# Kernel optimization log

Hardware: AMD Instinct MI355X
Metric: run time of the kernel (lower is better)

Reference implementation:

```python
import jax, jax.numpy as jnp
import numpy as np

D = 1024
H = 16
HD = D // H  # 64


def setup_inputs() -> dict:
    key = jax.random.key(0)
    k1, k2, k3 = jax.random.split(key, 3)
    x = jax.random.normal(k1, (2, 2048, D), dtype=jnp.float32)
    # fused QKV projection weight [d, 3d] and output projection [d, d], no bias
    Wqkv = jax.random.normal(k2, (D, 3 * D), dtype=jnp.float32) * (1.0 / np.sqrt(D))
    Wo = jax.random.normal(k3, (D, D), dtype=jnp.float32) * (1.0 / np.sqrt(D))
    return {"x": x, "Wqkv": Wqkv, "Wo": Wo}


def reference(x, Wqkv, Wo):
    b, t, d = x.shape
    qkv = x @ Wqkv  # [b, t, 3d]
    q, k, v = jnp.split(qkv, 3, axis=-1)
    # [b, t, d] -> [b, h, t, hd]
    def heads(z):
        return z.reshape(b, t, H, HD).transpose(0, 2, 1, 3)
    q, k, v = heads(q), heads(k), heads(v)
    scale = 1.0 / np.sqrt(HD)
    att = jnp.einsum('bhqd,bhkd->bhqk', q, k) * scale  # [b, h, t, t]
    att = jax.nn.softmax(att, axis=-1)
    y = jnp.einsum('bhqk,bhkd->bhqd', att, v)  # [b, h, t, hd]
    y = y.transpose(0, 2, 1, 3).reshape(b, t, d)  # [b, t, d]
    return y @ Wo
```

## Files before the change

### kernel.cpp

```cpp
#include <hip/hip_runtime.h>
#include <hip/hip_bf16.h>

#define D_MODEL 1024
#define NHEADS  16
#define HD      64
#define BATCH   2
#define SEQ     2048
#define NTOK    (BATCH * SEQ)

typedef __attribute__((ext_vector_type(8))) short bf16x8;
typedef __attribute__((ext_vector_type(4))) float f32x4;

#if __has_builtin(__builtin_amdgcn_exp2f)
#define EXP2F(x) __builtin_amdgcn_exp2f(x)
#else
#define EXP2F(x) exp2f(x)
#endif

static __device__ __forceinline__ short f2bf(float f) {
    union { float f; unsigned u; } x; x.f = f;
    unsigned r = (x.u + 0x7fffu + ((x.u >> 16) & 1u)) >> 16;
    return (short)r;
}

static __device__ __forceinline__ unsigned pk_bf16(float a, float b) {
    __hip_bfloat162 h2 = __float22bfloat162_rn(make_float2(a, b));
    union { __hip_bfloat162 h; unsigned u; } c; c.h = h2;
    return c.u;
}

static __device__ __forceinline__ void gl_lds16(const short* g, short* l) {
    __builtin_amdgcn_global_load_lds((const __attribute__((address_space(1))) void*)g,
                                     (__attribute__((address_space(3))) void*)l,
                                     16, 0, 0);
}

__global__ __launch_bounds__(256) void prep_kernel(const float* __restrict__ x,
                                                   short* __restrict__ x_bf,
                                                   const float* __restrict__ Wqkv,
                                                   short* __restrict__ WqkvT,
                                                   const float* __restrict__ Wo,
                                                   short* __restrict__ WoT,
                                                   float cexp) {
    int bid = blockIdx.x;
    int tid = threadIdx.x;

    if (bid < 4096) {
        int i = bid * 256 + tid;
        float4 v = ((const float4*)x)[i];
        short4 o;
        o.x = f2bf(v.x); o.y = f2bf(v.y); o.z = f2bf(v.z); o.w = f2bf(v.w);
        ((short4*)x_bf)[i] = o;
        return;
    }

    __shared__ float tile[32][33];
    const float* in; short* out; int R, C, slimit; float sc; int bx, by;
    if (bid < 4096 + 3072) {
        int idx = bid - 4096;
        in = Wqkv; out = WqkvT; R = D_MODEL; C = 3 * D_MODEL;
        slimit = D_MODEL; sc = cexp;
        bx = idx % 96; by = idx / 96;
    } else {
        int idx = bid - 7168;
        in = Wo; out = WoT; R = D_MODEL; C = D_MODEL;
        slimit = 0; sc = 1.0f;
        bx = idx % 32; by = idx / 32;
    }
    int bc = bx * 32, br = by * 32;
    int tx = tid & 31, ty = tid >> 5;
    #pragma unroll
    for (int i = 0; i < 32; i += 8)
        tile[ty + i][tx] = in[(long)(br + ty + i) * C + bc + tx];
    __syncthreads();
    #pragma unroll
    for (int i = 0; i < 32; i += 8) {
        int orow = bc + ty + i;
        float v = tile[tx][ty + i];
        if (orow < slimit) v *= sc;
        out[(long)orow * R + br + tx] = f2bf(v);
    }
}

__global__ __launch_bounds__(256) void gemm_out(const short* __restrict__ A,
                                                const short* __restrict__ BT,
                                                float* __restrict__ C,
                                                int M, int N, int K) {
    __shared__ short As[2][128 * 32];
    __shared__ short Bs[2][64 * 32];

    int tid  = threadIdx.x;
    int lane = tid & 63;
    int w    = tid >> 6;
    int quad = lane >> 4;
    int l16  = lane & 15;

    int m_blk = blockIdx.y * 128, n_blk = blockIdx.x * 64;

    const short* Ag = A  + (long)(m_blk + w * 32 + (lane >> 2)) * K + (lane & 3) * 8;
    const short* Bg = BT + (long)(n_blk + w * 16 + (lane >> 2)) * K + (lane & 3) * 8;
    short* As0 = &As[0][(w * 32) * 32];
    short* As1 = &As[1][(w * 32) * 32];
    short* Bs0 = &Bs[0][(w * 16) * 32];
    short* Bs1 = &Bs[1][(w * 16) * 32];

    f32x4 acc[2][4] = {};

    for (int k0 = 0; k0 < K; k0 += 64) {
        __syncthreads();
        gl_lds16(Ag + k0,               As0);
        gl_lds16(Ag + 16 * K + k0,      As0 + 16 * 32);
        gl_lds16(Ag + k0 + 32,          As1);
        gl_lds16(Ag + 16 * K + k0 + 32, As1 + 16 * 32);
        gl_lds16(Bg + k0,               Bs0);
        gl_lds16(Bg + k0 + 32,          Bs1);
        __syncthreads();

        #pragma unroll
        for (int kk = 0; kk < 2; kk++) {
            bf16x8 a[2], b[4];
            #pragma unroll
            for (int i = 0; i < 2; i++)
                a[i] = *(const bf16x8*)&As[kk][(w * 32 + i * 16 + l16) * 32 + quad * 8];
            #pragma unroll
            for (int j = 0; j < 4; j++)
                b[j] = *(const bf16x8*)&Bs[kk][(j * 16 + l16) * 32 + quad * 8];
            #pragma unroll
            for (int i = 0; i < 2; i++)
                #pragma unroll
                for (int j = 0; j < 4; j++)
                    acc[i][j] = __builtin_amdgcn_mfma_f32_16x16x32_bf16(a[i], b[j], acc[i][j], 0, 0, 0);
        }
    }

    #pragma unroll
    for (int i = 0; i < 2; i++)
        #pragma unroll
        for (int j = 0; j < 4; j++)
            #pragma unroll
            for (int r = 0; r < 4; r++) {
                int row = m_blk + w * 32 + i * 16 + quad * 4 + r;
                int col = n_blk + j * 16 + l16;
                C[(long)row * N + col] = acc[i][j][r];
            }
}

__global__ __launch_bounds__(256) void gemm_qkv(const short* __restrict__ A,
                                                const short* __restrict__ BT,
                                                short* __restrict__ Qb,
                                                short* __restrict__ Kt2,
                                                short* __restrict__ Vt2) {
    const int K = 1024;
    __shared__ union {
        struct { short As[2][128 * 32]; short Bs[2][128 * 32]; } g;
        short Tl[4][64][72];
    } sh;

    int tid  = threadIdx.x;
    int lane = tid & 63;
    int w    = tid >> 6;
    int quad = lane >> 4;
    int l16  = lane & 15;

    int bid = blockIdx.y * 24 + blockIdx.x;
    int xcd = bid & 7;
    int pos = bid >> 3;
    int nb  = xcd * 3 + (pos % 3);
    int mb  = pos / 3;

    int m_blk = mb * 128, n_blk = nb * 128;
    int mh = (w >> 1) * 64, nh = (w & 1) * 64;

    int sel = nb >> 3;
    int ncol0 = n_blk - sel * 1024;

    const short* Ag = A  + (long)(m_blk + w * 32 + (lane >> 2)) * K + (lane & 3) * 8;
    const short* Bg = BT + (long)(n_blk + w * 32 + (lane >> 2)) * K + (lane & 3) * 8;
    short* As0 = &sh.g.As[0][(w * 32) * 32];
    short* As1 = &sh.g.As[1][(w * 32) * 32];
    short* Bs0 = &sh.g.Bs[0][(w * 32) * 32];
    short* Bs1 = &sh.g.Bs[1][(w * 32) * 32];

    f32x4 acc[4][4] = {};

    for (int k0 = 0; k0 < K; k0 += 64) {
        __syncthreads();
        gl_lds16(Ag + k0,               As0);
        gl_lds16(Ag + 16 * K + k0,      As0 + 16 * 32);
        gl_lds16(Ag + k0 + 32,          As1);
        gl_lds16(Ag + 16 * K + k0 + 32, As1 + 16 * 32);
        gl_lds16(Bg + k0,               Bs0);
        gl_lds16(Bg + 16 * K + k0,      Bs0 + 16 * 32);
        gl_lds16(Bg + k0 + 32,          Bs1);
        gl_lds16(Bg + 16 * K + k0 + 32, Bs1 + 16 * 32);
        __syncthreads();

        #pragma unroll
        for (int kk = 0; kk < 2; kk++) {
            bf16x8 a[4], b[4];
            #pragma unroll
            for (int i = 0; i < 4; i++)
                a[i] = *(const bf16x8*)&sh.g.As[kk][(mh + i * 16 + l16) * 32 + quad * 8];
            #pragma unroll
            for (int j = 0; j < 4; j++)
                b[j] = *(const bf16x8*)&sh.g.Bs[kk][(nh + j * 16 + l16) * 32 + quad * 8];
            #pragma unroll
            for (int i = 0; i < 4; i++)
                #pragma unroll
                for (int j = 0; j < 4; j++)
                    acc[i][j] = __builtin_amdgcn_mfma_f32_16x16x32_bf16(a[i], b[j], acc[i][j], 0, 0, 0);
        }
    }

    __syncthreads();

    #pragma unroll
    for (int i = 0; i < 4; i++)
        #pragma unroll
        for (int j = 0; j < 4; j++)
            #pragma unroll
            for (int r = 0; r < 4; r++)
                sh.Tl[w][i * 16 + quad * 4 + r][j * 16 + l16] = f2bf(acc[i][j][r]);

    int R0q = m_blk + mh;
    if (sel == 0) {
        long qbase = (long)R0q * 1024 + (ncol0 + nh);
        #pragma unroll
        for (int ch = 0; ch < 8; ch++) {
            int row  = ch * 8 + (lane >> 3);
            int col0 = (lane & 7) * 8;
            *(bf16x8*)(Qb + qbase + (long)row * 1024 + col0) =
                *(const bf16x8*)&sh.Tl[w][row][col0];
        }
    } else {
        int b2 = R0q >> 11;
        int t  = (R0q & 2047) >> 6;
        int h  = (ncol0 + nh) >> 6;
        long obase = (long)(b2 * 16 + h) * (SEQ * 64) + (long)t * 4096;
        short* outT = (sel == 1) ? Kt2 : Vt2;
        if (sel == 1) {
            #pragma unroll
            for (int ch = 0; ch < 8; ch++) {
                int o = lane * 64 + ch * 8;
                int u = o >> 9, qd = (o >> 7) & 3, l = (o >> 3) & 15;
                int row = (u >> 2) * 32 + ((u >> 1) & 1) * 16 + l;
                int col = (u & 1) * 32 + qd * 8;
                *(bf16x8*)(outT + obase + o) = *(const bf16x8*)&sh.Tl[w][row][col];
            }
        } else {
            #pragma unroll
            for (int ch = 0; ch < 8; ch++) {
                int o = lane * 64 + ch * 8;
                int c = o >> 11, j2 = (o >> 9) & 3, qd = (o >> 7) & 3, l = (o >> 3) & 15;
                int hd = j2 * 16 + l;
                bf16x8 ov;
                #pragma unroll
                for (int jj = 0; jj < 8; jj++) {
                    int s = c * 32 + qd * 8 + jj;
                    int key = (s >> 2) + ((s & 3) << 4);
                    ov[jj] = sh.Tl[w][key][hd];
                }
                *(bf16x8*)(outT + obase + o) = ov;
            }
        }
    }
}

__global__ __launch_bounds__(256, 4) void flash_attn(const short* __restrict__ Qb,
                                                     const short* __restrict__ Kt2,
                                                     const short* __restrict__ Vt2,
                                                     short* __restrict__ y) {
    int tid  = threadIdx.x;
    int lane = tid & 63;
    int w    = tid >> 6;
    int quad = lane >> 4;
    int l16  = lane & 15;
    int qsel = w & 1;
    int ksel = w >> 1;

    int bh = blockIdx.y;
    int b  = bh >> 4;
    int h  = bh & 15;
    int qw = blockIdx.x * 64 + qsel * 32;

    __shared__ union {
        short Ps[4][32 * 72];
        float Mg[2][64][41];
    } sh;
    short* PsW = &sh.Ps[w][0];

    const short* Qrow = Qb + ((long)b * SEQ + qw + l16) * 1024 + h * 64;
    bf16x8 aQ[2][2];
    #pragma unroll
    for (int m = 0; m < 2; m++)
        #pragma unroll
        for (int c = 0; c < 2; c++)
            aQ[m][c] = *(const bf16x8*)(Qrow + (long)(m * 16) * 1024 + c * 32 + quad * 8);

    const short* Ktb = Kt2 + (long)bh * (SEQ * 64) + (long)ksel * 16 * 4096;
    const short* Vtb = Vt2 + (long)bh * (SEQ * 64) + (long)ksel * 16 * 4096;

    f32x4 O[2][4] = {};
    f32x4 Lacc[2] = {};
    bf16x8 ones;
    #pragma unroll
    for (int i = 0; i < 8; i++) ones[i] = (short)0x3F80;

    for (int t = 0; t < 16; t++) {
        const short* Kt = Ktb + t * 4096;
        const short* Vt = Vtb + t * 4096;

        bf16x8 kf[8];
        #pragma unroll
        for (int u = 0; u < 8; u++) kf[u] = *(const bf16x8*)(Kt + u * 512 + lane * 8);

        f32x4 z[2][4];
        #pragma unroll
        for (int m = 0; m < 2; m++)
            #pragma unroll
            for (int kc = 0; kc < 4; kc++) {
                f32x4 zz = {};
                zz = __builtin_amdgcn_mfma_f32_16x16x32_bf16(aQ[m][0], kf[2 * kc],     zz, 0, 0, 0);
                z[m][kc] = __builtin_amdgcn_mfma_f32_16x16x32_bf16(aQ[m][1], kf[2 * kc + 1], zz, 0, 0, 0);
            }

        bf16x8 vf[8];
        #pragma unroll
        for (int u = 0; u < 8; u++) vf[u] = *(const bf16x8*)(Vt + u * 512 + lane * 8);

        #pragma unroll
        for (int m = 0; m < 2; m++)
            #pragma unroll
            for (int r = 0; r < 4; r++) {
                unsigned d0 = pk_bf16(EXP2F(z[m][0][r]), EXP2F(z[m][1][r]));
                unsigned d1 = pk_bf16(EXP2F(z[m][2][r]), EXP2F(z[m][3][r]));
                unsigned long long dd = ((unsigned long long)d1 << 32) | d0;
                *(unsigned long long*)((unsigned*)PsW + (m * 16 + quad * 4 + r) * 36 + 2 * l16) = dd;
            }

        #pragma unroll
        for (int c = 0; c < 2; c++) {
            bf16x8 aP0 = *(const bf16x8*)(PsW + (l16) * 72      + c * 32 + quad * 8);
            bf16x8 aP1 = *(const bf16x8*)(PsW + (16 + l16) * 72 + c * 32 + quad * 8);
            Lacc[0] = __builtin_amdgcn_mfma_f32_16x16x32_bf16(aP0, ones, Lacc[0], 0, 0, 0);
            Lacc[1] = __builtin_amdgcn_mfma_f32_16x16x32_bf16(aP1, ones, Lacc[1], 0, 0, 0);
            #pragma unroll
            for (int j = 0; j < 4; j++) {
                O[0][j] = __builtin_amdgcn_mfma_f32_16x16x32_bf16(aP0, vf[c * 4 + j], O[0][j], 0, 0, 0);
                O[1][j] = __builtin_amdgcn_mfma_f32_16x16x32_bf16(aP1, vf[c * 4 + j], O[1][j], 0, 0, 0);
            }
        }
    }

    __syncthreads();
    if (ksel) {
        float* mg = &sh.Mg[qsel][lane][0];
        #pragma unroll
        for (int m = 0; m < 2; m++)
            #pragma unroll
            for (int j = 0; j < 4; j++)
                #pragma unroll
                for (int r = 0; r < 4; r++)
                    mg[m * 16 + j * 4 + r] = O[m][j][r];
        #pragma unroll
        for (int m = 0; m < 2; m++)
            #pragma unroll
            for (int r = 0; r < 4; r++)
                mg[32 + m * 4 + r] = Lacc[m][r];
    }
    __syncthreads();
    if (!ksel) {
        const float* mg = &sh.Mg[qsel][lane][0];
        #pragma unroll
        for (int m = 0; m < 2; m++)
            #pragma unroll
            for (int j = 0; j < 4; j++)
                #pragma unroll
                for (int r = 0; r < 4; r++)
                    O[m][j][r] += mg[m * 16 + j * 4 + r];
        #pragma unroll
        for (int m = 0; m < 2; m++)
            #pragma unroll
            for (int r = 0; r < 4; r++)
                Lacc[m][r] += mg[32 + m * 4 + r];

        #pragma unroll
        for (int m = 0; m < 2; m++) {
            f32x4 rl;
            #pragma unroll
            for (int r = 0; r < 4; r++) rl[r] = 1.0f / Lacc[m][r];
            #pragma unroll
            for (int j = 0; j < 4; j++)
                #pragma unroll
                for (int r = 0; r < 4; r++) {
                    int row = qw + m * 16 + quad * 4 + r;
                    y[((long)b * SEQ + row) * D_MODEL + h * HD + j * 16 + l16] =
                        f2bf(O[m][j][r] * rl[r]);
                }
        }
    }
}

extern "C" void kernel_launch(void* const* d_in, const int* in_sizes, int n_in,
                              void* d_out, int out_size, void* d_ws, size_t ws_size,
                              hipStream_t stream) {
    const float* x    = (const float*)d_in[0];
    const float* Wqkv = (const float*)d_in[1];
    const float* Wo   = (const float*)d_in[2];

    char* ws = (char*)d_ws;
    short* Qb    = (short*)(ws);
    short* Kt2   = (short*)(ws + 25165824);
    short* Vt2   = (short*)(ws + 33554432);
    short* WqkvT = (short*)(ws + 41943040);
    short* WoT   = (short*)(ws + 48234496);
    short* x_bf  = (short*)d_out;
    short* yb    = (short*)(ws + 8388608);

    const float cexp = 0.125f * 1.4426950408889634f;

    prep_kernel<<<8192, 256, 0, stream>>>(x, x_bf, Wqkv, WqkvT, Wo, WoT, cexp);

    gemm_qkv<<<dim3(3 * D_MODEL / 128, NTOK / 128), 256, 0, stream>>>(
        x_bf, WqkvT, Qb, Kt2, Vt2);

    flash_attn<<<dim3(SEQ / 64, BATCH * NHEADS), 256, 0, stream>>>(Qb, Kt2, Vt2, yb);

    gemm_out<<<dim3(D_MODEL / 64, NTOK / 128), 256, 0, stream>>>(
        yb, WoT, (float*)d_out, NTOK, D_MODEL, D_MODEL);
}
```

Measured before the change: 188.3 us.

## Give each attention wave full key range over 16 queries, prefetch next K tile

Each wave now owns 16 query rows and walks all 32 key tiles itself, instead of pairs of waves splitting the key range over 32 rows. This removes the LDS merge of partial outputs and row sums, the two block barriers, and the union shared buffer. It also software-prefetches the next K tile into registers while the current tile's softmax and PV run. In exchange, each K/V fragment loaded from global memory is reused by half as many query rows per wave, so K/V traffic per query rises. The last iteration's prefetch reads one tile past the head's K data.

Result: slower. 200.3 us (+6.4%).

```diff
diff --git a/kernel.cpp b/kernel.cpp
--- a/kernel.cpp
+++ b/kernel.cpp
@@ -275,130 +275,81 @@
     int w    = tid >> 6;
     int quad = lane >> 4;
     int l16  = lane & 15;
-    int qsel = w & 1;
-    int ksel = w >> 1;
 
     int bh = blockIdx.y;
     int b  = bh >> 4;
     int h  = bh & 15;
-    int qw = blockIdx.x * 64 + qsel * 32;
-
-    __shared__ union {
-        short Ps[4][32 * 72];
-        float Mg[2][64][41];
-    } sh;
-    short* PsW = &sh.Ps[w][0];
+    int qw = blockIdx.x * 64 + w * 16;
+
+    __shared__ short Ps[4][16 * 72];
+    short* PsW = &Ps[w][0];
 
     const short* Qrow = Qb + ((long)b * SEQ + qw + l16) * 1024 + h * 64;
-    bf16x8 aQ[2][2];
-    #pragma unroll
-    for (int m = 0; m < 2; m++)
-        #pragma unroll
-        for (int c = 0; c < 2; c++)
-            aQ[m][c] = *(const bf16x8*)(Qrow + (long)(m * 16) * 1024 + c * 32 + quad * 8);
-
-    const short* Ktb = Kt2 + (long)bh * (SEQ * 64) + (long)ksel * 16 * 4096;
-    const short* Vtb = Vt2 + (long)bh * (SEQ * 64) + (long)ksel * 16 * 4096;
-
-    f32x4 O[2][4] = {};
-    f32x4 Lacc[2] = {};
+    bf16x8 aQ[2];
+    #pragma unroll
+    for (int c = 0; c < 2; c++)
+        aQ[c] = *(const bf16x8*)(Qrow + c * 32 + quad * 8);
+
+    const short* Ktb = Kt2 + (long)bh * (SEQ * 64);
+    const short* Vtb = Vt2 + (long)bh * (SEQ * 64);
+
+    f32x4 O[4] = {};
+    f32x4 Lacc = {};
     bf16x8 ones;
     #pragma unroll
     for (int i = 0; i < 8; i++) ones[i] = (short)0x3F80;
 
-    for (int t = 0; t < 16; t++) {
-        const short* Kt = Ktb + t * 4096;
-        const short* Vt = Vtb + t * 4096;
-
-        bf16x8 kf[8];
-        #pragma unroll
-        for (int u = 0; u < 8; u++) kf[u] = *(const bf16x8*)(Kt + u * 512 + lane * 8);
-
-        f32x4 z[2][4];
-        #pragma unroll
-        for (int m = 0; m < 2; m++)
-            #pragma unroll
-            for (int kc = 0; kc < 4; kc++) {
-                f32x4 zz = {};
-                zz = __builtin_amdgcn_mfma_f32_16x16x32_bf16(aQ[m][0], kf[2 * kc],     zz, 0, 0, 0);
-                z[m][kc] = __builtin_amdgcn_mfma_f32_16x16x32_bf16(aQ[m][1], kf[2 * kc + 1], zz, 0, 0, 0);
-            }
+    bf16x8 kf[8];
+    #pragma unroll
+    for (int u = 0; u < 8; u++) kf[u] = *(const bf16x8*)(Ktb + u * 512 + lane * 8);
+
+    for (int t = 0; t < 32; t++) {
+        const short* Vt  = Vtb + t * 4096;
+        const short* Ktn = Ktb + (t + 1) * 4096;
+
+        f32x4 z[4];
+        #pragma unroll
+        for (int kc = 0; kc < 4; kc++) {
+            f32x4 zz = {};
+            zz = __builtin_amdgcn_mfma_f32_16x16x32_bf16(aQ[0], kf[2 * kc],     zz, 0, 0, 0);
+            z[kc] = __builtin_amdgcn_mfma_f32_16x16x32_bf16(aQ[1], kf[2 * kc + 1], zz, 0, 0, 0);
+        }
 
         bf16x8 vf[8];
         #pragma unroll
         for (int u = 0; u < 8; u++) vf[u] = *(const bf16x8*)(Vt + u * 512 + lane * 8);
-
-        #pragma unroll
-        for (int m = 0; m < 2; m++)
-            #pragma unroll
-            for (int r = 0; r < 4; r++) {
-                unsigned d0 = pk_bf16(EXP2F(z[m][0][r]), EXP2F(z[m][1][r]));
-                unsigned d1 = pk_bf16(EXP2F(z[m][2][r]), EXP2F(z[m][3][r]));
-                unsigned long long dd = ((unsigned long long)d1 << 32) | d0;
-                *(unsigned long long*)((unsigned*)PsW + (m * 16 + quad * 4 + r) * 36 + 2 * l16) = dd;
-            }
+        #pragma unroll
+        for (int u = 0; u < 8; u++) kf[u] = *(const bf16x8*)(Ktn + u * 512 + lane * 8);
+
+        #pragma unroll
+        for (int r = 0; r < 4; r++) {
+            unsigned d0 = pk_bf16(EXP2F(z[0][r]), EXP2F(z[1][r]));
+            unsigned d1 = pk_bf16(EXP2F(z[2][r]), EXP2F(z[3][r]));
+            unsigned long long dd = ((unsigned long long)d1 << 32) | d0;
+            *(unsigned long long*)((unsigned*)PsW + (quad * 4 + r) * 36 + 2 * l16) = dd;
+        }
 
         #pragma unroll
         for (int c = 0; c < 2; c++) {
-            bf16x8 aP0 = *(const bf16x8*)(PsW + (l16) * 72      + c * 32 + quad * 8);
-            bf16x8 aP1 = *(const bf16x8*)(PsW + (16 + l16) * 72 + c * 32 + quad * 8);
-            Lacc[0] = __builtin_amdgcn_mfma_f32_16x16x32_bf16(aP0, ones, Lacc[0], 0, 0, 0);
-            Lacc[1] = __builtin_amdgcn_mfma_f32_16x16x32_bf16(aP1, ones, Lacc[1], 0, 0, 0);
-            #pragma unroll
-            for (int j = 0; j < 4; j++) {
-                O[0][j] = __builtin_amdgcn_mfma_f32_16x16x32_bf16(aP0, vf[c * 4 + j], O[0][j], 0, 0, 0);
-                O[1][j] = __builtin_amdgcn_mfma_f32_16x16x32_bf16(aP1, vf[c * 4 + j], O[1][j], 0, 0, 0);
-            }
-        }
-    }
-
-    __syncthreads();
-    if (ksel) {
-        float* mg = &sh.Mg[qsel][lane][0];
-        #pragma unroll
-        for (int m = 0; m < 2; m++)
+            bf16x8 aP = *(const bf16x8*)(PsW + l16 * 72 + c * 32 + quad * 8);
+            Lacc = __builtin_amdgcn_mfma_f32_16x16x32_bf16(aP, ones, Lacc, 0, 0, 0);
             #pragma unroll
             for (int j = 0; j < 4; j++)
-                #pragma unroll
-                for (int r = 0; r < 4; r++)
-                    mg[m * 16 + j * 4 + r] = O[m][j][r];
-        #pragma unroll
-        for (int m = 0; m < 2; m++)
-            #pragma unroll
-            for (int r = 0; r < 4; r++)
-                mg[32 + m * 4 + r] = Lacc[m][r];
-    }
-    __syncthreads();
-    if (!ksel) {
-        const float* mg = &sh.Mg[qsel][lane][0];
-        #pragma unroll
-        for (int m = 0; m < 2; m++)
-            #pragma unroll
-            for (int j = 0; j < 4; j++)
-                #pragma unroll
-                for (int r = 0; r < 4; r++)
-                    O[m][j][r] += mg[m * 16 + j * 4 + r];
-        #pragma unroll
-        for (int m = 0; m < 2; m++)
-            #pragma unroll
-            for (int r = 0; r < 4; r++)
-                Lacc[m][r] += mg[32 + m * 4 + r];
-
-        #pragma unroll
-        for (int m = 0; m < 2; m++) {
-            f32x4 rl;
-            #pragma unroll
-            for (int r = 0; r < 4; r++) rl[r] = 1.0f / Lacc[m][r];
-            #pragma unroll
-            for (int j = 0; j < 4; j++)
-                #pragma unroll
-                for (int r = 0; r < 4; r++) {
-                    int row = qw + m * 16 + quad * 4 + r;
-                    y[((long)b * SEQ + row) * D_MODEL + h * HD + j * 16 + l16] =
-                        f2bf(O[m][j][r] * rl[r]);
-                }
-        }
-    }
+                O[j] = __builtin_amdgcn_mfma_f32_16x16x32_bf16(aP, vf[c * 4 + j], O[j], 0, 0, 0);
+        }
+    }
+
+    f32x4 rl;
+    #pragma unroll
+    for (int r = 0; r < 4; r++) rl[r] = 1.0f / Lacc[r];
+    #pragma unroll
+    for (int j = 0; j < 4; j++)
+        #pragma unroll
+        for (int r = 0; r < 4; r++) {
+            int row = qw + quad * 4 + r;
+            y[((long)b * SEQ + row) * D_MODEL + h * HD + j * 16 + l16] =
+                f2bf(O[j][r] * rl[r]);
+        }
 }
 
 extern "C" void kernel_launch(void* const* d_in, const int* in_sizes, int n_in,
```

## Share double-buffered K/V tiles in LDS across four query warps per block

Applied to the files above, without the earlier changes.

The attention kernel drops the split-K arrangement, where two warps each covered half the keys and merged through shared memory. Each block now owns 128 queries, one 32-query slice per warp, and all warps sweep the full key range. K/V tiles are loaded cooperatively into double-buffered LDS with async global-to-LDS copies, so each tile is fetched once per block instead of once per warp. Blocks are also remapped to a 1D grid with an interleaved order, which may change how they spread across XCDs and caches. Costs: half as many blocks, a longer serial loop, and a barrier on every iteration.

After: 188.2 us. No clear change (-0.1%).

```diff
diff --git a/kernel.cpp b/kernel.cpp
--- a/kernel.cpp
+++ b/kernel.cpp
@@ -275,19 +275,18 @@
     int w    = tid >> 6;
     int quad = lane >> 4;
     int l16  = lane & 15;
-    int qsel = w & 1;
-    int ksel = w >> 1;
-
-    int bh = blockIdx.y;
-    int b  = bh >> 4;
-    int h  = bh & 15;
-    int qw = blockIdx.x * 64 + qsel * 32;
-
-    __shared__ union {
-        short Ps[4][32 * 72];
-        float Mg[2][64][41];
-    } sh;
-    short* PsW = &sh.Ps[w][0];
+
+    int bid0 = blockIdx.x;
+    int nid  = (bid0 & 7) * 64 + (bid0 >> 3);
+    int bh   = nid >> 4;
+    int b    = bh >> 4;
+    int h    = bh & 15;
+    int qw   = (nid & 15) * 128 + w * 32;
+
+    __shared__ short Ks[2][4096];
+    __shared__ short Vs[2][4096];
+    __shared__ short Ps[4][32 * 72];
+    short* PsW = &Ps[w][0];
 
     const short* Qrow = Qb + ((long)b * SEQ + qw + l16) * 1024 + h * 64;
     bf16x8 aQ[2][2];
@@ -297,8 +296,8 @@
         for (int c = 0; c < 2; c++)
             aQ[m][c] = *(const bf16x8*)(Qrow + (long)(m * 16) * 1024 + c * 32 + quad * 8);
 
-    const short* Ktb = Kt2 + (long)bh * (SEQ * 64) + (long)ksel * 16 * 4096;
-    const short* Vtb = Vt2 + (long)bh * (SEQ * 64) + (long)ksel * 16 * 4096;
+    const short* Ktb = Kt2 + (long)bh * (SEQ * 64);
+    const short* Vtb = Vt2 + (long)bh * (SEQ * 64);
 
     f32x4 O[2][4] = {};
     f32x4 Lacc[2] = {};
@@ -306,13 +305,33 @@
     #pragma unroll
     for (int i = 0; i < 8; i++) ones[i] = (short)0x3F80;
 
-    for (int t = 0; t < 16; t++) {
-        const short* Kt = Ktb + t * 4096;
-        const short* Vt = Vtb + t * 4096;
+    int soff = w * 1024 + lane * 8;
+
+    {
+        const short* ks = Ktb + soff;
+        const short* vs = Vtb + soff;
+        gl_lds16(ks,       &Ks[0][w * 1024]);
+        gl_lds16(ks + 512, &Ks[0][w * 1024 + 512]);
+        gl_lds16(vs,       &Vs[0][w * 1024]);
+        gl_lds16(vs + 512, &Vs[0][w * 1024 + 512]);
+    }
+    __syncthreads();
+
+    for (int t = 0; t < 32; t++) {
+        int cur = t & 1;
+
+        if (t < 31) {
+            const short* ks = Ktb + (t + 1) * 4096 + soff;
+            const short* vs = Vtb + (t + 1) * 4096 + soff;
+            gl_lds16(ks,       &Ks[cur ^ 1][w * 1024]);
+            gl_lds16(ks + 512, &Ks[cur ^ 1][w * 1024 + 512]);
+            gl_lds16(vs,       &Vs[cur ^ 1][w * 1024]);
+            gl_lds16(vs + 512, &Vs[cur ^ 1][w * 1024 + 512]);
+        }
 
         bf16x8 kf[8];
         #pragma unroll
-        for (int u = 0; u < 8; u++) kf[u] = *(const bf16x8*)(Kt + u * 512 + lane * 8);
+        for (int u = 0; u < 8; u++) kf[u] = *(const bf16x8*)&Ks[cur][u * 512 + lane * 8];
 
         f32x4 z[2][4];
         #pragma unroll
@@ -326,7 +345,7 @@
 
         bf16x8 vf[8];
         #pragma unroll
-        for (int u = 0; u < 8; u++) vf[u] = *(const bf16x8*)(Vt + u * 512 + lane * 8);
+        for (int u = 0; u < 8; u++) vf[u] = *(const bf16x8*)&Vs[cur][u * 512 + lane * 8];
 
         #pragma unroll
         for (int m = 0; m < 2; m++)
@@ -350,54 +369,23 @@
                 O[1][j] = __builtin_amdgcn_mfma_f32_16x16x32_bf16(aP1, vf[c * 4 + j], O[1][j], 0, 0, 0);
             }
         }
-    }
-
-    __syncthreads();
-    if (ksel) {
-        float* mg = &sh.Mg[qsel][lane][0];
-        #pragma unroll
-        for (int m = 0; m < 2; m++)
-            #pragma unroll
-            for (int j = 0; j < 4; j++)
-                #pragma unroll
-                for (int r = 0; r < 4; r++)
-                    mg[m * 16 + j * 4 + r] = O[m][j][r];
-        #pragma unroll
-        for (int m = 0; m < 2; m++)
-            #pragma unroll
-            for (int r = 0; r < 4; r++)
-                mg[32 + m * 4 + r] = Lacc[m][r];
-    }
-    __syncthreads();
-    if (!ksel) {
-        const float* mg = &sh.Mg[qsel][lane][0];
-        #pragma unroll
-        for (int m = 0; m < 2; m++)
-            #pragma unroll
-            for (int j = 0; j < 4; j++)
-                #pragma unroll
-                for (int r = 0; r < 4; r++)
-                    O[m][j][r] += mg[m * 16 + j * 4 + r];
-        #pragma unroll
-        for (int m = 0; m < 2; m++)
-            #pragma unroll
-            for (int r = 0; r < 4; r++)
-                Lacc[m][r] += mg[32 + m * 4 + r];
-
-        #pragma unroll
-        for (int m = 0; m < 2; m++) {
-            f32x4 rl;
-            #pragma unroll
-            for (int r = 0; r < 4; r++) rl[r] = 1.0f / Lacc[m][r];
-            #pragma unroll
-            for (int j = 0; j < 4; j++)
-                #pragma unroll
-                for (int r = 0; r < 4; r++) {
-                    int row = qw + m * 16 + quad * 4 + r;
-                    y[((long)b * SEQ + row) * D_MODEL + h * HD + j * 16 + l16] =
-                        f2bf(O[m][j][r] * rl[r]);
-                }
-        }
+
+        __syncthreads();
+    }
+
+    #pragma unroll
+    for (int m = 0; m < 2; m++) {
+        f32x4 rl;
+        #pragma unroll
+        for (int r = 0; r < 4; r++) rl[r] = 1.0f / Lacc[m][r];
+        #pragma unroll
+        for (int j = 0; j < 4; j++)
+            #pragma unroll
+            for (int r = 0; r < 4; r++) {
+                int row = qw + m * 16 + quad * 4 + r;
+                y[((long)b * SEQ + row) * D_MODEL + h * HD + j * 16 + l16] =
+                    f2bf(O[m][j][r] * rl[r]);
+            }
     }
 }
 
@@ -424,7 +412,7 @@
     gemm_qkv<<<dim3(3 * D_MODEL / 128, NTOK / 128), 256, 0, stream>>>(
         x_bf, WqkvT, Qb, Kt2, Vt2);
 
-    flash_attn<<<dim3(SEQ / 64, BATCH * NHEADS), 256, 0, stream>>>(Qb, Kt2, Vt2, yb);
+    flash_attn<<<512, 256, 0, stream>>>(Qb, Kt2, Vt2, yb);
 
     gemm_out<<<dim3(D_MODEL / 64, NTOK / 128), 256, 0, stream>>>(
         yb, WoT, (float*)d_out, NTOK, D_MODEL, D_MODEL);
```
